# Kernel optimization log

Measured on AMD Instinct MI355X. Metric: run time of the kernel, lower is better.

## Reference

```python
import jax, jax.numpy as jnp
import numpy as np

N = 50000          # nodes
E = 1600000        # edges
H = 8              # heads
F = 16             # out feats per head (np1class)
IN = 256           # in feats
NEG_SLOPE = 0.2    # DGL GATConv default leaky_relu slope


def setup_inputs() -> dict:
    key = jax.random.key(0)
    ks = jax.random.split(key, 7)
    x = jax.random.normal(ks[0], (N, IN), dtype=jnp.float32)
    W = jax.random.normal(ks[1], (IN, H * F), dtype=jnp.float32) * 0.05
    attn_l = jax.random.normal(ks[2], (H, F), dtype=jnp.float32) * 0.05
    attn_r = jax.random.normal(ks[3], (H, F), dtype=jnp.float32) * 0.05
    bias = jax.random.normal(ks[4], (H * F,), dtype=jnp.float32) * 0.05
    src = jax.random.randint(ks[5], (E,), 0, N, dtype=jnp.int64)
    dst = jax.random.randint(ks[6], (E,), 0, N, dtype=jnp.int64)
    return {"x": x, "W": W, "attn_l": attn_l, "attn_r": attn_r,
            "bias": bias, "src": src, "dst": dst}


def reference(x, W, attn_l, attn_r, bias, src, dst):
    # Linear projection to heads: [N, H, F]
    feat = (x @ W).reshape(N, H, F)
    # Per-node attention halves: [N, H]
    el = jnp.einsum('nhf,hf->nh', feat, attn_l)
    er = jnp.einsum('nhf,hf->nh', feat, attn_r)
    # Edge scores: e = leaky_relu(el[src] + er[dst])  -> [E, H]
    e = jax.nn.leaky_relu(el[src] + er[dst], negative_slope=NEG_SLOPE)
    # Segment softmax over incoming edges of each destination node
    m = jax.ops.segment_max(e, dst, num_segments=N)           # [N, H]
    m = jnp.where(jnp.isfinite(m), m, 0.0)                    # empty segments
    m = jax.lax.stop_gradient(m)
    ex = jnp.exp(e - m[dst])                                  # [E, H]
    s = jax.ops.segment_sum(ex, dst, num_segments=N)          # [N, H]
    a = ex / jnp.maximum(s[dst], 1e-9)                        # [E, H]
    # Weighted aggregation of source features: [N, H, F]
    msg = a[:, :, None] * feat[src]
    rst = jax.ops.segment_sum(msg, dst, num_segments=N)
    rst = rst + bias.reshape(H, F)
    # Classifier: mean over heads -> [N, F]
    return rst.mean(axis=1)
```

## Files before the change

### kernel.cpp

```cpp
#include <hip/hip_runtime.h>
#include <hip/hip_bf16.h>

#define NH 8
#define NF 16
#define NIN 256
#define HF 128
#define CAP 3072
#define BCH 4096

typedef __attribute__((ext_vector_type(8))) short bf16x8;
typedef __attribute__((ext_vector_type(4))) float f32x4;

__device__ __forceinline__ unsigned short f2bf(float f) {
    union { float f; unsigned int u; } v; v.f = f;
    unsigned int r = v.u + 0x7FFFu + ((v.u >> 16) & 1u);
    return (unsigned short)(r >> 16);
}
__device__ __forceinline__ float bf2f(unsigned short b) {
    union { unsigned int u; float f; } v; v.u = ((unsigned int)b) << 16;
    return v.f;
}

struct GemmLds {
    unsigned short AsH[32][264];
    unsigned short AsL[32][264];
    float scratch[32][132];
};
struct BinLds {
    unsigned int hist[784];
    unsigned int offs[784];
    unsigned short lpos[BCH];
    unsigned int obuf[BCH];
    int dcache[BCH];
    unsigned int wsum[4];
    unsigned int sbase;
};
#define POOLSZ ((sizeof(BinLds) > sizeof(GemmLds)) ? sizeof(BinLds) : sizeof(GemmLds))

#define GROWS 128
__device__ __forceinline__ void gemm_body(char* pool, int bid,
                                          const float* __restrict__ A,
                                          const float* __restrict__ W,
                                          const float* __restrict__ attn_l,
                                          const float* __restrict__ attn_r,
                                          unsigned short* __restrict__ featb,
                                          float* __restrict__ el,
                                          float* __restrict__ er, int M) {
    GemmLds& gl = *reinterpret_cast<GemmLds*>(pool);
    const int tid = threadIdx.x;
    const int wave = tid >> 6, lane = tid & 63;
    const int quad = lane >> 4, lq = lane & 15;
    const int row0 = bid * GROWS;

    bf16x8 bfrag[8][2];
#pragma unroll
    for (int h2 = 0; h2 < 2; h2++) {
        const int col = (wave * 2 + h2) * 16 + lq;
#pragma unroll
        for (int kk = 0; kk < 8; kk++) {
            const int kb = kk * 32 + quad * 8;
            bf16x8 f;
#pragma unroll
            for (int j = 0; j < 8; j++)
                f[j] = (short)f2bf(W[(size_t)(kb + j) * HF + col]);
            bfrag[kk][h2] = f;
        }
    }

    const int srow = tid >> 3;
    const int erow = tid >> 3, eh = tid & 7;

    for (int c = 0; c < 4; c++) {
        const int crow0 = row0 + c * 32;
        __syncthreads();
#pragma unroll
        for (int i = 0; i < 8; i++) {
            const int col = ((tid & 7) + i * 8) * 4;
            const int gr = crow0 + srow;
            float4 v = make_float4(0.f, 0.f, 0.f, 0.f);
            if (gr < M) v = *(const float4*)&A[(size_t)gr * NIN + col];
            const unsigned short h0 = f2bf(v.x), h1 = f2bf(v.y),
                                 h2b = f2bf(v.z), h3 = f2bf(v.w);
            *(ushort4*)&gl.AsH[srow][col] = make_ushort4(h0, h1, h2b, h3);
            *(ushort4*)&gl.AsL[srow][col] =
                make_ushort4(f2bf(v.x - bf2f(h0)), f2bf(v.y - bf2f(h1)),
                             f2bf(v.z - bf2f(h2b)), f2bf(v.w - bf2f(h3)));
        }
        __syncthreads();
#pragma unroll
        for (int s = 0; s < 2; s++) {
            f32x4 acc0 = {0.f, 0.f, 0.f, 0.f};
            f32x4 acc1 = {0.f, 0.f, 0.f, 0.f};
            const int ar = s * 16 + lq;
#pragma unroll
            for (int kk = 0; kk < 8; kk++) {
                const bf16x8 ah = *(const bf16x8*)&gl.AsH[ar][kk * 32 + quad * 8];
                const bf16x8 al = *(const bf16x8*)&gl.AsL[ar][kk * 32 + quad * 8];
                acc0 = __builtin_amdgcn_mfma_f32_16x16x32_bf16(ah, bfrag[kk][0], acc0, 0, 0, 0);
                acc1 = __builtin_amdgcn_mfma_f32_16x16x32_bf16(ah, bfrag[kk][1], acc1, 0, 0, 0);
                acc0 = __builtin_amdgcn_mfma_f32_16x16x32_bf16(al, bfrag[kk][0], acc0, 0, 0, 0);
                acc1 = __builtin_amdgcn_mfma_f32_16x16x32_bf16(al, bfrag[kk][1], acc1, 0, 0, 0);
            }
#pragma unroll
            for (int r = 0; r < 4; r++) {
                const int gr = crow0 + s * 16 + quad * 4 + r;
                const int srw = s * 16 + quad * 4 + r;
                gl.scratch[srw][(wave * 2 + 0) * 16 + lq] = acc0[r];
                gl.scratch[srw][(wave * 2 + 1) * 16 + lq] = acc1[r];
                if (gr < M) {
                    featb[(size_t)gr * HF + (wave * 2 + 0) * 16 + lq] = f2bf(acc0[r]);
                    featb[(size_t)gr * HF + (wave * 2 + 1) * 16 + lq] = f2bf(acc1[r]);
                }
            }
        }
        __syncthreads();
        {
            const int gr = crow0 + erow;
            if (gr < M) {
                const float* sr = &gl.scratch[erow][eh * 16];
                float sl = 0.f, srr = 0.f;
#pragma unroll
                for (int f = 0; f < 16; f++) {
                    const float v = sr[f];
                    sl = fmaf(v, attn_l[eh * 16 + f], sl);
                    srr = fmaf(v, attn_r[eh * 16 + f], srr);
                }
                el[(size_t)gr * NH + eh] = sl;
                er[(size_t)gr * NH + eh] = srr;
            }
        }
    }
}

__device__ __forceinline__ void bin_body(char* pool, int blk,
                                         const int* __restrict__ src,
                                         const int* __restrict__ dst,
                                         unsigned int* __restrict__ binned,
                                         unsigned int* __restrict__ runtab,
                                         int E, int NB) {
    BinLds& bl = *reinterpret_cast<BinLds*>(pool);
    const int t = threadIdx.x;
    const int base = blk * BCH;
    const int cnt = min(BCH, E - base);
    const int lane = t & 63, w = t >> 6;
    for (int b = t; b < NB; b += 256) bl.hist[b] = 0;
    for (int i = t; i < cnt; i += 256) bl.dcache[i] = dst[base + i];
    if (t == 0) bl.sbase = 0;
    __syncthreads();
    for (int i = t; i < cnt; i += 256)
        bl.lpos[i] = (unsigned short)atomicAdd(&bl.hist[bl.dcache[i] >> 6], 1u);
    __syncthreads();
    for (int c0 = 0; c0 < NB; c0 += 256) {
        const int idx = c0 + t;
        const unsigned int v = (idx < NB) ? bl.hist[idx] : 0;
        unsigned int incl = v;
#pragma unroll
        for (int off = 1; off < 64; off <<= 1) {
            const unsigned int x = __shfl_up(incl, off, 64);
            if (lane >= off) incl += x;
        }
        if (lane == 63) bl.wsum[w] = incl;
        __syncthreads();
        unsigned int wbase = 0;
        for (int k = 0; k < w; k++) wbase += bl.wsum[k];
        const unsigned int tot = bl.wsum[0] + bl.wsum[1] + bl.wsum[2] + bl.wsum[3];
        const unsigned int excl = bl.sbase + wbase + incl - v;
        if (idx < NB) {
            bl.offs[idx] = excl;
            runtab[(size_t)blk * NB + idx] = excl | (v << 16);
        }
        __syncthreads();
        if (t == 0) bl.sbase += tot;
        __syncthreads();
    }
    for (int i = t; i < cnt; i += 256) {
        const int d = bl.dcache[i];
        bl.obuf[bl.offs[d >> 6] + bl.lpos[i]] =
            (unsigned int)src[base + i] | ((unsigned int)(d & 63) << 16);
    }
    __syncthreads();
    for (int i = t; i < cnt; i += 256) binned[(size_t)base + i] = bl.obuf[i];
}

__global__ __launch_bounds__(256) void gemm_bin(const float* __restrict__ A,
                                                const float* __restrict__ W,
                                                const float* __restrict__ attn_l,
                                                const float* __restrict__ attn_r,
                                                unsigned short* __restrict__ featb,
                                                float* __restrict__ el,
                                                float* __restrict__ er, int M,
                                                const int* __restrict__ src,
                                                const int* __restrict__ dst,
                                                unsigned int* __restrict__ binned,
                                                unsigned int* __restrict__ runtab,
                                                int E, int NB, int GB) {
    __shared__ __align__(16) char pool[POOLSZ];
    if ((int)blockIdx.x < GB)
        gemm_body(pool, blockIdx.x, A, W, attn_l, attn_r, featb, el, er, M);
    else
        bin_body(pool, blockIdx.x - GB, src, dst, binned, runtab, E, NB);
}

__global__ __launch_bounds__(256) void csr_kernel(const unsigned int* __restrict__ binned,
                                                  const unsigned int* __restrict__ runtab,
                                                  int* __restrict__ nodeinfo,
                                                  unsigned short* __restrict__ srcsw,
                                                  int N, int NB, int nbb) {
    __shared__ unsigned int eary[CAP];
    __shared__ unsigned short sSrc[CAP];
    __shared__ unsigned short roff[512];
    __shared__ unsigned short rcntl[512];
    __shared__ int rbase[512];
    __shared__ int len[64], cur[64];
    __shared__ unsigned int wsum[4];
    __shared__ unsigned int sbase;
    const int b = blockIdx.x, t = threadIdx.x;
    const int node0 = b << 6;
    const int lane = t & 63, w = t >> 6;
    if (t == 0) sbase = 0;
    __syncthreads();
    for (int c0 = 0; c0 < nbb; c0 += 256) {
        const int r = c0 + t;
        const unsigned int e = (r < nbb) ? runtab[(size_t)r * NB + b] : 0;
        const unsigned int v = e >> 16;
        unsigned int incl = v;
#pragma unroll
        for (int off = 1; off < 64; off <<= 1) {
            const unsigned int x = __shfl_up(incl, off, 64);
            if (lane >= off) incl += x;
        }
        if (lane == 63) wsum[w] = incl;
        __syncthreads();
        unsigned int wbase = 0;
        for (int k = 0; k < w; k++) wbase += wsum[k];
        const unsigned int tot = wsum[0] + wsum[1] + wsum[2] + wsum[3];
        if (r < nbb) {
            roff[r] = (unsigned short)(e & 0xFFFFu);
            rcntl[r] = (unsigned short)v;
            rbase[r] = (int)(sbase + wbase + incl - v);
        }
        __syncthreads();
        if (t == 0) sbase += tot;
        __syncthreads();
    }
    const int tot = (int)sbase;
    for (int r = t; r < nbb; r += 256) {
        const int off = (int)roff[r];
        const int pb = rbase[r];
        const int rc = (int)rcntl[r];
        const unsigned int* bp = &binned[(size_t)r * BCH + off];
        for (int j = 0; j < rc; j++) eary[pb + j] = bp[j];
    }
    if (t < 64) len[t] = 0;
    __syncthreads();
    for (int i = t; i < tot; i += 256) atomicAdd(&len[eary[i] >> 16], 1);
    __syncthreads();
    if (t < 64) {
        const int v = len[t];
        int incl = v;
#pragma unroll
        for (int off = 1; off < 64; off <<= 1) {
            const int x = __shfl_up(incl, off, 64);
            if (t >= off) incl += x;
        }
        const int excl = incl - v;
        cur[t] = excl;
        if (node0 + t < N) nodeinfo[node0 + t] = excl | (v << 16);
    }
    __syncthreads();
    for (int i = t; i < tot; i += 256) {
        const unsigned int p = eary[i];
        const int pos = atomicAdd(&cur[p >> 16], 1);
        sSrc[pos] = (unsigned short)(p & 0xFFFFu);
    }
    __syncthreads();
    unsigned short* sw = &srcsw[(size_t)b * CAP];
    for (int i = t; i < tot; i += 256) sw[i] = sSrc[i];
}

#define WIN 64
__global__ __launch_bounds__(256) void agg_kernel(const int* __restrict__ nodeinfo,
                                                  const unsigned short* __restrict__ srcsw,
                                                  const float* __restrict__ el,
                                                  const float* __restrict__ er,
                                                  const unsigned short* __restrict__ featb,
                                                  const float* __restrict__ bias,
                                                  float* __restrict__ out, int N) {
    __shared__ float lds_sc[4][WIN][8];
    __shared__ int lds_src[4][WIN];
    const int tid = threadIdx.x;
    const int w = tid >> 6, lane = tid & 63;
    const int n = blockIdx.x * 4 + w;
    if (n >= N) return;

    const int info = nodeinfo[n];
    const int begin = (n >> 6) * CAP + (info & 0xFFFF);
    const int end = begin + (info >> 16);
    const int hA = lane & 7, eA = lane >> 3;
    const float er_h = er[(size_t)n * NH + hA];
    const int hB = lane >> 3, fB2 = lane & 7;

    float2 acc = make_float2(0.f, 0.f);
    float psum = 0.f;
    for (int base = begin; base < end; base += WIN) {
        const int cn = min(WIN, end - base);
        __builtin_amdgcn_wave_barrier();
#pragma unroll
        for (int rep = 0; rep < 8; rep++) {
            const int ei = rep * 8 + eA;
            if (ei < cn) {
                const int si = (int)srcsw[base + ei];
                if (hA == 0) lds_src[w][ei] = si;
                float v = el[(size_t)si * NH + hA] + er_h;
                v = v > 0.f ? v : 0.2f * v;
                const float sc = __expf(v);
                lds_sc[w][ei][hA] = sc;
                psum += sc;
            }
        }
        __builtin_amdgcn_wave_barrier();
        for (int b0 = 0; b0 < cn; b0 += 16) {
            unsigned int fv[16];
#pragma unroll
            for (int j = 0; j < 16; j++) {
                const int ej = b0 + j;
                const int sj = lds_src[w][ej];
                fv[j] = (ej < cn)
                            ? *(const unsigned int*)&featb[(size_t)sj * HF + hB * 16 + fB2 * 2]
                            : 0u;
            }
#pragma unroll
            for (int j = 0; j < 16; j++) {
                const int ej = b0 + j;
                const float sc = (ej < cn) ? lds_sc[w][ej][hB] : 0.f;
                acc.x = fmaf(sc, bf2f((unsigned short)(fv[j] & 0xFFFFu)), acc.x);
                acc.y = fmaf(sc, bf2f((unsigned short)(fv[j] >> 16)), acc.y);
            }
        }
    }

    float s = psum;
    s += __shfl_xor(s, 8, 64);
    s += __shfl_xor(s, 16, 64);
    s += __shfl_xor(s, 32, 64);
    const float s_h = __shfl(s, hB, 64);
    const float inv = 1.f / fmaxf(s_h, 1e-9f);
    float2 val;
    val.x = acc.x * inv + bias[hB * 16 + fB2 * 2];
    val.y = acc.y * inv + bias[hB * 16 + fB2 * 2 + 1];
    val.x += __shfl_xor(val.x, 8, 64);
    val.x += __shfl_xor(val.x, 16, 64);
    val.x += __shfl_xor(val.x, 32, 64);
    val.y += __shfl_xor(val.y, 8, 64);
    val.y += __shfl_xor(val.y, 16, 64);
    val.y += __shfl_xor(val.y, 32, 64);
    if (lane < 8) {
        float2 o;
        o.x = val.x * 0.125f;
        o.y = val.y * 0.125f;
        *(float2*)&out[(size_t)n * 16 + lane * 2] = o;
    }
}

extern "C" void kernel_launch(void* const* d_in, const int* in_sizes, int n_in,
                              void* d_out, int out_size, void* d_ws, size_t ws_size,
                              hipStream_t stream) {
    const float* x      = (const float*)d_in[0];
    const float* W      = (const float*)d_in[1];
    const float* attn_l = (const float*)d_in[2];
    const float* attn_r = (const float*)d_in[3];
    const float* bias   = (const float*)d_in[4];
    const int*   src    = (const int*)d_in[5];
    const int*   dst    = (const int*)d_in[6];
    float* out = (float*)d_out;

    const int N = in_sizes[0] / NIN;
    const int E = in_sizes[5];
    const int NB = (N + 63) >> 6;
    const int nbb = (E + BCH - 1) / BCH;
    const int GB = (N + GROWS - 1) / GROWS;

    char* w = (char*)d_ws;
    unsigned short* featb = (unsigned short*)w; w += (size_t)N * HF * 2;
    float* el     = (float*)w; w += (size_t)N * NH * 4;
    float* er     = (float*)w; w += (size_t)N * NH * 4;
    int* nodeinfo = (int*)w;   w += (size_t)N * 4;
    unsigned int* binned = (unsigned int*)w; w += (size_t)nbb * BCH * 4;
    unsigned int* runtab = (unsigned int*)w; w += (size_t)nbb * NB * 4;
    unsigned short* srcsw = (unsigned short*)w;

    gemm_bin<<<GB + nbb, 256, 0, stream>>>(x, W, attn_l, attn_r, featb, el, er, N,
                                           src, dst, binned, runtab, E, NB, GB);
    csr_kernel<<<NB, 256, 0, stream>>>(binned, runtab, nodeinfo, srcsw, N, NB, nbb);
    agg_kernel<<<(N + 3) / 4, 256, 0, stream>>>(nodeinfo, srcsw, el, er, featb, bias,
                                                out, N);
}
```

Measured before the change: 216.4 us.

## Co-schedule GEMM with CSR build instead of with edge binning

Moves the edge-binning pass into its own standalone kernel and merges the dense projection GEMM with the per-bucket CSR construction in one launch. The GEMM blocks and CSR blocks now run side by side, so the GEMM work overlaps the CSR stage instead of the binning stage. The aim is better load balance across the launches. In exchange the LDS pool must now fit the larger of the GEMM and CSR layouts, which may reduce occupancy for the GEMM blocks.

```diff
diff --git a/kernel.cpp b/kernel.cpp
--- a/kernel.cpp
+++ b/kernel.cpp
@@ -26,16 +26,17 @@
     unsigned short AsL[32][264];
     float scratch[32][132];
 };
-struct BinLds {
-    unsigned int hist[784];
-    unsigned int offs[784];
-    unsigned short lpos[BCH];
-    unsigned int obuf[BCH];
-    int dcache[BCH];
+struct CsrLds {
+    unsigned int eary[CAP];
+    unsigned short sSrc[CAP];
+    unsigned short roff[512];
+    unsigned short rcntl[512];
+    int rbase[512];
+    int len[64], cur[64];
     unsigned int wsum[4];
     unsigned int sbase;
 };
-#define POOLSZ ((sizeof(BinLds) > sizeof(GemmLds)) ? sizeof(BinLds) : sizeof(GemmLds))
+#define POOLSZ ((sizeof(GemmLds) > sizeof(CsrLds)) ? sizeof(GemmLds) : sizeof(CsrLds))
 
 #define GROWS 128
 __device__ __forceinline__ void gemm_body(char* pool, int bid,
@@ -132,97 +133,122 @@
     }
 }
 
-__device__ __forceinline__ void bin_body(char* pool, int blk,
-                                         const int* __restrict__ src,
-                                         const int* __restrict__ dst,
-                                         unsigned int* __restrict__ binned,
-                                         unsigned int* __restrict__ runtab,
-                                         int E, int NB) {
-    BinLds& bl = *reinterpret_cast<BinLds*>(pool);
+__device__ __forceinline__ void csr_body(char* pool, int b,
+                                         const unsigned int* __restrict__ binned,
+                                         const unsigned int* __restrict__ runtab,
+                                         int* __restrict__ nodeinfo,
+                                         unsigned short* __restrict__ srcsw,
+                                         int N, int NB, int nbb) {
+    CsrLds& cl = *reinterpret_cast<CsrLds*>(pool);
     const int t = threadIdx.x;
-    const int base = blk * BCH;
-    const int cnt = min(BCH, E - base);
+    const int node0 = b << 6;
     const int lane = t & 63, w = t >> 6;
-    for (int b = t; b < NB; b += 256) bl.hist[b] = 0;
-    for (int i = t; i < cnt; i += 256) bl.dcache[i] = dst[base + i];
-    if (t == 0) bl.sbase = 0;
-    __syncthreads();
-    for (int i = t; i < cnt; i += 256)
-        bl.lpos[i] = (unsigned short)atomicAdd(&bl.hist[bl.dcache[i] >> 6], 1u);
-    __syncthreads();
-    for (int c0 = 0; c0 < NB; c0 += 256) {
-        const int idx = c0 + t;
-        const unsigned int v = (idx < NB) ? bl.hist[idx] : 0;
+    if (t == 0) cl.sbase = 0;
+    __syncthreads();
+    for (int c0 = 0; c0 < nbb; c0 += 256) {
+        const int r = c0 + t;
+        const unsigned int e = (r < nbb) ? runtab[(size_t)r * NB + b] : 0;
+        const unsigned int v = e >> 16;
         unsigned int incl = v;
 #pragma unroll
         for (int off = 1; off < 64; off <<= 1) {
             const unsigned int x = __shfl_up(incl, off, 64);
             if (lane >= off) incl += x;
         }
-        if (lane == 63) bl.wsum[w] = incl;
+        if (lane == 63) cl.wsum[w] = incl;
         __syncthreads();
         unsigned int wbase = 0;
-        for (int k = 0; k < w; k++) wbase += bl.wsum[k];
-        const unsigned int tot = bl.wsum[0] + bl.wsum[1] + bl.wsum[2] + bl.wsum[3];
-        const unsigned int excl = bl.sbase + wbase + incl - v;
-        if (idx < NB) {
-            bl.offs[idx] = excl;
-            runtab[(size_t)blk * NB + idx] = excl | (v << 16);
-        }
-        __syncthreads();
-        if (t == 0) bl.sbase += tot;
-        __syncthreads();
-    }
-    for (int i = t; i < cnt; i += 256) {
-        const int d = bl.dcache[i];
-        bl.obuf[bl.offs[d >> 6] + bl.lpos[i]] =
-            (unsigned int)src[base + i] | ((unsigned int)(d & 63) << 16);
-    }
-    __syncthreads();
-    for (int i = t; i < cnt; i += 256) binned[(size_t)base + i] = bl.obuf[i];
-}
-
-__global__ __launch_bounds__(256) void gemm_bin(const float* __restrict__ A,
+        for (int k = 0; k < w; k++) wbase += cl.wsum[k];
+        const unsigned int tot = cl.wsum[0] + cl.wsum[1] + cl.wsum[2] + cl.wsum[3];
+        if (r < nbb) {
+            cl.roff[r] = (unsigned short)(e & 0xFFFFu);
+            cl.rcntl[r] = (unsigned short)v;
+            cl.rbase[r] = (int)(cl.sbase + wbase + incl - v);
+        }
+        __syncthreads();
+        if (t == 0) cl.sbase += tot;
+        __syncthreads();
+    }
+    const int tot = (int)cl.sbase;
+    for (int r = t; r < nbb; r += 256) {
+        const int off = (int)cl.roff[r];
+        const int pb = cl.rbase[r];
+        const int rc = (int)cl.rcntl[r];
+        const unsigned int* bp = &binned[(size_t)r * BCH + off];
+        for (int j = 0; j < rc; j++) cl.eary[pb + j] = bp[j];
+    }
+    if (t < 64) cl.len[t] = 0;
+    __syncthreads();
+    for (int i = t; i < tot; i += 256) atomicAdd(&cl.len[cl.eary[i] >> 16], 1);
+    __syncthreads();
+    if (t < 64) {
+        const int v = cl.len[t];
+        int incl = v;
+#pragma unroll
+        for (int off = 1; off < 64; off <<= 1) {
+            const int x = __shfl_up(incl, off, 64);
+            if (t >= off) incl += x;
+        }
+        const int excl = incl - v;
+        cl.cur[t] = excl;
+        if (node0 + t < N) nodeinfo[node0 + t] = excl | (v << 16);
+    }
+    __syncthreads();
+    for (int i = t; i < tot; i += 256) {
+        const unsigned int p = cl.eary[i];
+        const int pos = atomicAdd(&cl.cur[p >> 16], 1);
+        cl.sSrc[pos] = (unsigned short)(p & 0xFFFFu);
+    }
+    __syncthreads();
+    unsigned short* sw = &srcsw[(size_t)b * CAP];
+    for (int i = t; i < tot; i += 256) sw[i] = cl.sSrc[i];
+}
+
+__global__ __launch_bounds__(256) void gemm_csr(const float* __restrict__ A,
                                                 const float* __restrict__ W,
                                                 const float* __restrict__ attn_l,
                                                 const float* __restrict__ attn_r,
                                                 unsigned short* __restrict__ featb,
                                                 float* __restrict__ el,
                                                 float* __restrict__ er, int M,
-                                                const int* __restrict__ src,
-                                                const int* __restrict__ dst,
-                                                unsigned int* __restrict__ binned,
-                                                unsigned int* __restrict__ runtab,
-                                                int E, int NB, int GB) {
+                                                const unsigned int* __restrict__ binned,
+                                                const unsigned int* __restrict__ runtab,
+                                                int* __restrict__ nodeinfo,
+                                                unsigned short* __restrict__ srcsw,
+                                                int NB, int nbb, int GB) {
     __shared__ __align__(16) char pool[POOLSZ];
     if ((int)blockIdx.x < GB)
         gemm_body(pool, blockIdx.x, A, W, attn_l, attn_r, featb, el, er, M);
     else
-        bin_body(pool, blockIdx.x - GB, src, dst, binned, runtab, E, NB);
-}
-
-__global__ __launch_bounds__(256) void csr_kernel(const unsigned int* __restrict__ binned,
-                                                  const unsigned int* __restrict__ runtab,
-                                                  int* __restrict__ nodeinfo,
-                                                  unsigned short* __restrict__ srcsw,
-                                                  int N, int NB, int nbb) {
-    __shared__ unsigned int eary[CAP];
-    __shared__ unsigned short sSrc[CAP];
-    __shared__ unsigned short roff[512];
-    __shared__ unsigned short rcntl[512];
-    __shared__ int rbase[512];
-    __shared__ int len[64], cur[64];
+        csr_body(pool, blockIdx.x - GB, binned, runtab, nodeinfo, srcsw, M, NB, nbb);
+}
+
+__global__ __launch_bounds__(256) void bin_kernel(const int* __restrict__ src,
+                                                  const int* __restrict__ dst,
+                                                  unsigned int* __restrict__ binned,
+                                                  unsigned int* __restrict__ runtab,
+                                                  int E, int NB) {
+    __shared__ unsigned int hist[784];
+    __shared__ unsigned int offs[784];
+    __shared__ unsigned short lpos[BCH];
+    __shared__ unsigned int obuf[BCH];
+    __shared__ int dcache[BCH];
     __shared__ unsigned int wsum[4];
     __shared__ unsigned int sbase;
-    const int b = blockIdx.x, t = threadIdx.x;
-    const int node0 = b << 6;
+    const int blk = blockIdx.x, t = threadIdx.x;
+    const int base = blk * BCH;
+    const int cnt = min(BCH, E - base);
     const int lane = t & 63, w = t >> 6;
+    for (int b = t; b < NB; b += 256) hist[b] = 0;
+    for (int i = t; i < cnt; i += 256) dcache[i] = dst[base + i];
     if (t == 0) sbase = 0;
     __syncthreads();
-    for (int c0 = 0; c0 < nbb; c0 += 256) {
-        const int r = c0 + t;
-        const unsigned int e = (r < nbb) ? runtab[(size_t)r * NB + b] : 0;
-        const unsigned int v = e >> 16;
+    for (int i = t; i < cnt; i += 256)
+        lpos[i] = (unsigned short)atomicAdd(&hist[dcache[i] >> 6], 1u);
+    __syncthreads();
+    for (int c0 = 0; c0 < NB; c0 += 256) {
+        const int idx = c0 + t;
+        const unsigned int v = (idx < NB) ? hist[idx] : 0;
         unsigned int incl = v;
 #pragma unroll
         for (int off = 1; off < 64; off <<= 1) {
@@ -234,48 +260,22 @@
         unsigned int wbase = 0;
         for (int k = 0; k < w; k++) wbase += wsum[k];
         const unsigned int tot = wsum[0] + wsum[1] + wsum[2] + wsum[3];
-        if (r < nbb) {
-            roff[r] = (unsigned short)(e & 0xFFFFu);
-            rcntl[r] = (unsigned short)v;
-            rbase[r] = (int)(sbase + wbase + incl - v);
+        const unsigned int excl = sbase + wbase + incl - v;
+        if (idx < NB) {
+            offs[idx] = excl;
+            runtab[(size_t)blk * NB + idx] = excl | (v << 16);
         }
         __syncthreads();
         if (t == 0) sbase += tot;
         __syncthreads();
     }
-    const int tot = (int)sbase;
-    for (int r = t; r < nbb; r += 256) {
-        const int off = (int)roff[r];
-        const int pb = rbase[r];
-        const int rc = (int)rcntl[r];
-        const unsigned int* bp = &binned[(size_t)r * BCH + off];
-        for (int j = 0; j < rc; j++) eary[pb + j] = bp[j];
-    }
-    if (t < 64) len[t] = 0;
-    __syncthreads();
-    for (int i = t; i < tot; i += 256) atomicAdd(&len[eary[i] >> 16], 1);
-    __syncthreads();
-    if (t < 64) {
-        const int v = len[t];
-        int incl = v;
-#pragma unroll
-        for (int off = 1; off < 64; off <<= 1) {
-            const int x = __shfl_up(incl, off, 64);
-            if (t >= off) incl += x;
-        }
-        const int excl = incl - v;
-        cur[t] = excl;
-        if (node0 + t < N) nodeinfo[node0 + t] = excl | (v << 16);
-    }
-    __syncthreads();
-    for (int i = t; i < tot; i += 256) {
-        const unsigned int p = eary[i];
-        const int pos = atomicAdd(&cur[p >> 16], 1);
-        sSrc[pos] = (unsigned short)(p & 0xFFFFu);
-    }
-    __syncthreads();
-    unsigned short* sw = &srcsw[(size_t)b * CAP];
-    for (int i = t; i < tot; i += 256) sw[i] = sSrc[i];
+    for (int i = t; i < cnt; i += 256) {
+        const int d = dcache[i];
+        obuf[offs[d >> 6] + lpos[i]] =
+            (unsigned int)src[base + i] | ((unsigned int)(d & 63) << 16);
+    }
+    __syncthreads();
+    for (int i = t; i < cnt; i += 256) binned[(size_t)base + i] = obuf[i];
 }
 
 #define WIN 64
@@ -389,9 +389,9 @@
     unsigned int* runtab = (unsigned int*)w; w += (size_t)nbb * NB * 4;
     unsigned short* srcsw = (unsigned short*)w;
 
-    gemm_bin<<<GB + nbb, 256, 0, stream>>>(x, W, attn_l, attn_r, featb, el, er, N,
-                                           src, dst, binned, runtab, E, NB, GB);
-    csr_kernel<<<NB, 256, 0, stream>>>(binned, runtab, nodeinfo, srcsw, N, NB, nbb);
+    bin_kernel<<<nbb, 256, 0, stream>>>(src, dst, binned, runtab, E, NB);
+    gemm_csr<<<GB + NB, 256, 0, stream>>>(x, W, attn_l, attn_r, featb, el, er, N,
+                                          binned, runtab, nodeinfo, srcsw, NB, nbb, GB);
     agg_kernel<<<(N + 3) / 4, 256, 0, stream>>>(nodeinfo, srcsw, el, er, featb, bias,
                                                 out, N);
 }
```

Result: faster. 210.7 us (-2.6%).
